# Kernel tuning notes

Hardware: AMD Instinct MI355X
Metric: run time of the kernel (lower is better)

The kernel has to match this reference:

```python
import jax, jax.numpy as jnp
import numpy as np

B, C, E, K, HW = 8, 64, 4, 2, 128
LEAK = 0.2      # LeakyReLU slope in gate and experts
CLAMP = 0.8     # InvBlock clamp
EPS = 1e-5      # InstanceNorm eps


def _conv(x, w, b, pad):
    # x: [B,Ci,H,W], w: [Co,Ci,kh,kw] (OIHW)
    y = jax.lax.conv_general_dilated(x, w, (1, 1), [(pad, pad), (pad, pad)],
                                     dimension_numbers=('NCHW', 'OIHW', 'NCHW'))
    return y + b[None, :, None, None]


def _inorm(x, g, b):
    # InstanceNorm2d: per-sample, per-channel over H,W; biased variance
    m = x.mean(axis=(2, 3), keepdims=True)
    v = x.var(axis=(2, 3), keepdims=True)
    return (x - m) / jnp.sqrt(v + EPS) * g[None, :, None, None] + b[None, :, None, None]


def _hin(x, w1, b1, nw, nb, w2, b2):
    # HinResBlock with relu_slope=1 (d=1 passed by InvBlock) -> activations are identity
    r = _conv(x, w1, b1, 1)
    h1, h2 = jnp.split(r, 2, axis=1)
    r = jnp.concatenate([_inorm(h1, nw, nb), h2], axis=1)
    r = _conv(r, w2, b2, 1)
    return x + r


def setup_inputs() -> dict:
    key = jax.random.key(0)
    ks = jax.random.split(key, 20)
    s = 0.05
    Ch = C // 2
    inp = {
        'x': jax.random.normal(ks[0], (B, 2 * C, HW, HW), jnp.float32),
        # invertible 1x1 conv weight [2C, 2C]
        'winv': jax.random.normal(ks[1], (2 * C, 2 * C), jnp.float32) * s,
        # stacked HinResBlock params for F (idx 0), G (idx 1), H (idx 2)
        'blk_w1': jax.random.normal(ks[2], (3, C, C, 3, 3), jnp.float32) * s,
        'blk_b1': jax.random.normal(ks[3], (3, C), jnp.float32) * s,
        'blk_nw': jnp.ones((3, Ch), jnp.float32),
        'blk_nb': jnp.zeros((3, Ch), jnp.float32),
        'blk_w2': jax.random.normal(ks[4], (3, C, C, 3, 3), jnp.float32) * s,
        'blk_b2': jax.random.normal(ks[5], (3, C), jnp.float32) * s,
        # fuse 1x1 conv 2C -> C
        'fuse_w': jax.random.normal(ks[6], (C, 2 * C, 1, 1), jnp.float32) * s,
        'fuse_b': jax.random.normal(ks[7], (C,), jnp.float32) * s,
        # gate: fc0 (noise) random; fc1 weight zero-init per source, bias random
        'gw0': jax.random.normal(ks[8], (E, C), jnp.float32) * s,
        'gb0': jax.random.normal(ks[9], (E,), jnp.float32) * s,
        'gw1': jnp.zeros((E, C), jnp.float32),
        'gb1': jax.random.normal(ks[10], (E,), jnp.float32) * s,
        # stacked expert ConvProce params
        'ew1': jax.random.normal(ks[11], (E, C, C, 3, 3), jnp.float32) * s,
        'eb1': jax.random.normal(ks[12], (E, C), jnp.float32) * s,
        'ew2': jax.random.normal(ks[13], (E, C, C, 3, 3), jnp.float32) * s,
        'eb2': jax.random.normal(ks[14], (E, C), jnp.float32) * s,
    }
    return inp


def _forward(x, winv, blk_w1, blk_b1, blk_nw, blk_nb, blk_w2, blk_b2,
             fuse_w, fuse_b, gw0, gb0, gw1, gb1, ew1, eb1, ew2, eb2):
    # --- pre_fuse: InvBlock(2C, C) then 1x1 conv 2C->C ---
    z = jnp.einsum('oi,bihw->bohw', winv, x)  # invertible 1x1 conv (logdet unused)
    x1, x2 = z[:, :C], z[:, C:]
    hin = lambda i, h: _hin(h, blk_w1[i], blk_b1[i], blk_nw[i], blk_nb[i], blk_w2[i], blk_b2[i])
    y1 = x1 + hin(0, x2)                         # F
    s = CLAMP * (jax.nn.sigmoid(hin(2, y1)) * 2.0 - 1.0)  # H
    y2 = x2 * jnp.exp(s) + hin(1, y1)            # G
    xf = _conv(jnp.concatenate([y1, y2], axis=1), fuse_w, fuse_b, 0)  # [B,C,H,W]

    # --- gate ---
    g = jnp.max(xf, axis=(2, 3)) + jnp.mean(xf, axis=(2, 3))  # [B,C]
    lg = jax.nn.leaky_relu(g @ gw1.T + gb1, LEAK)             # [B,E]
    noise = jax.nn.softplus(g @ gw0.T + gb0)
    nm = noise.mean(axis=1, keepdims=True)
    ns = jnp.std(noise, axis=1, ddof=1, keepdims=True)        # torch.std is unbiased
    norm_noise = (noise - nm) / ns
    _, idx = jax.lax.top_k(lg + norm_noise, K)                # [B,K]
    mask = jnp.zeros((B, E), lg.dtype).at[jnp.arange(B)[:, None], idx].set(1.0)
    cof = jax.nn.softmax(jnp.where(mask > 0, lg, -jnp.inf), axis=1)  # [B,E]

    # --- experts: dense weighted combine (non-topk gates are exactly 0) ---
    def expert(w1, b1, w2, b2):
        h = jax.nn.leaky_relu(_conv(xf, w1, b1, 1), LEAK)
        return _conv(h, w2, b2, 1) + xf
    eouts = jax.vmap(expert)(ew1, eb1, ew2, eb2)  # [E,B,C,H,W]
    out = jnp.einsum('ebchw,be->bchw', eouts, cof)
    return out, cof


def reference(x, winv, blk_w1, blk_b1, blk_nw, blk_nb, blk_w2, blk_b2,
              fuse_w, fuse_b, gw0, gb0, gw1, gb1, ew1, eb1, ew2, eb2):
    return _forward(x, winv, blk_w1, blk_b1, blk_nw, blk_nb, blk_w2, blk_b2,
                    fuse_w, fuse_b, gw0, gb0, gw1, gb1, ew1, eb1, ew2, eb2)
```

## Files before the change

### kernel.cpp

```cpp
#include <hip/hip_runtime.h>
#include <cstddef>


#define HW2 16384
typedef short short8 __attribute__((ext_vector_type(8)));
typedef float f32x4 __attribute__((ext_vector_type(4)));
typedef unsigned short ushort_t;
typedef unsigned int uint_t;

enum { M_PLAIN = 0, M_ADD2 = 1, M_SIGEXP = 2, M_COUPLE = 3, M_LRELU = 4 };

__device__ __forceinline__ float bf2f(ushort_t u) {
  return __uint_as_float(((uint_t)u) << 16);
}
__device__ __forceinline__ ushort_t f2bf(float f) {
  uint_t u = __float_as_uint(f);
  u += 0x7fffu + ((u >> 16) & 1u);
  return (ushort_t)(u >> 16);
}
__device__ __forceinline__ uint_t pack2(float a, float b) {
  return (uint_t)f2bf(a) | ((uint_t)f2bf(b) << 16);
}
__device__ __forceinline__ void ld4bf(const ushort_t* p, float* o) {
  uint2 d = *(const uint2*)p;
  o[0] = bf2f((ushort_t)(d.x & 0xffff)); o[1] = bf2f((ushort_t)(d.x >> 16));
  o[2] = bf2f((ushort_t)(d.y & 0xffff)); o[3] = bf2f((ushort_t)(d.y >> 16));
}
__device__ __forceinline__ void st4bf(ushort_t* p, const float* v) {
  uint2 st; st.x = pack2(v[0], v[1]); st.y = pack2(v[2], v[3]);
  *(uint2*)p = st;
}
__device__ __forceinline__ void gload_lds16(const void* g, void* l) {
  __builtin_amdgcn_global_load_lds(
      (const __attribute__((address_space(1))) void*)g,
      (__attribute__((address_space(3))) void*)l, 16, 0, 0);
}

__global__ void wtrans_kernel(const float* __restrict__ bw1, const float* __restrict__ bw2,
                              const float* __restrict__ ew1, const float* __restrict__ ew2,
                              ushort_t* __restrict__ wbuf) {
  int idx = blockIdx.x * 256 + threadIdx.x;
  int ci = idx & 63; int co = (idx >> 6) & 63;
  int rest = idx >> 12;
  int tap = rest % 9; int conv = rest / 9;
  const float* src;
  if (conv < 3)       src = bw1 + (size_t)conv * 36864;
  else if (conv < 6)  src = bw2 + (size_t)(conv - 3) * 36864;
  else if (conv < 10) src = ew1 + (size_t)(conv - 6) * 36864;
  else                src = ew2 + (size_t)(conv - 10) * 36864;
  float v = src[(co * 64 + ci) * 9 + tap];
  int n = co >> 4, col = co & 15;
  int h = ci >> 5, krow = (ci >> 3) & 3, e = ci & 7;
  int pos = conv * 36864 + (((tap * 2 + h) * 4 + n) << 9) + ((col << 2) + krow) * 8 + e;
  wbuf[pos] = f2bf(v);
}

__global__ void cvt_kernel(const float* __restrict__ s, ushort_t* __restrict__ d, int n) {
  int i = blockIdx.x * 256 + threadIdx.x;
  if (i < n) d[i] = f2bf(s[i]);
}

__global__ __launch_bounds__(256) void xtrans_kernel(const float* __restrict__ x,
                                                     ushort_t* __restrict__ xh) {
  int b = blockIdx.y;
  int oct = blockIdx.x >> 6;
  int p = ((blockIdx.x & 63) << 8) + threadIdx.x;
  short8 v;
#pragma unroll
  for (int j = 0; j < 8; ++j)
    v[j] = (short)f2bf(x[((size_t)(b * 128 + oct * 8 + j)) * HW2 + p]);
  *(short8*)(xh + ((size_t)b * HW2 + p) * 128 + oct * 8) = v;
}

template <int MODE, bool INORM>
__global__ __launch_bounds__(256, 2) void conv3_kernel(
    const ushort_t* __restrict__ in, int icstr, int icoff,
    const ushort_t* __restrict__ wgt, const float* __restrict__ bias,
    void* __restrict__ outv, int ocstr, int ocoff,
    const ushort_t* __restrict__ r1, int r1cstr, int r1off,
    const ushort_t* __restrict__ r2, int r2cstr, int r2off,
    const ushort_t* __restrict__ mul, int mcstr, int moff,
    const float* __restrict__ kh, const int* __restrict__ eidx) {
  int b = blockIdx.y;
  if (MODE == M_LRELU) {
    int e = eidx[b * 2 + (int)blockIdx.z];
    wgt += (size_t)(6 + e) * 36864;
    bias += e * 64;
    outv = (void*)((ushort_t*)outv + (size_t)blockIdx.z * 8388608);
  }
  int tile = blockIdx.x;
  int ty0 = (tile >> 3) << 4;
  int tx0 = (tile & 7) << 4;
  int t = threadIdx.x;
  int lane = t & 63, w = t >> 6;

  __shared__ __align__(16) ushort_t sm[2592 * 8];
  char* smb = (char*)sm;

  if (!INORM) {
    for (int j = t; j < 2592; j += 256) {
      int row = j / 144, rem = j - row * 144;
      int xx = rem >> 3;
      int gy = ty0 + row - 1, gx = tx0 + xx - 1;
      if ((unsigned)gy >= 128u || (unsigned)gx >= 128u) {
        short8 z = {0, 0, 0, 0, 0, 0, 0, 0};
        *(short8*)(smb + (j << 4)) = z;
      }
    }
    for (int k = w; k < 41; k += 4) {
      int j = (k << 6) + lane;
      int row = j / 144, rem = j - row * 144;
      int xx = rem >> 3, octS = rem & 7;
      int oct = octS ^ (xx & 7);
      int gy = ty0 + row - 1, gx = tx0 + xx - 1;
      if (j < 2592 && (unsigned)gy < 128u && (unsigned)gx < 128u) {
        const ushort_t* gp =
            in + ((size_t)b * HW2 + (gy << 7) + gx) * icstr + icoff + oct * 8;
        gload_lds16(gp, smb + (k << 10));
      }
    }
  } else {
    short8 v[11];
#pragma unroll
    for (int k = 0; k < 11; ++k) {
      int j = t + (k << 8);
      short8 vv = {0, 0, 0, 0, 0, 0, 0, 0};
      if (j < 2592) {
        int row = j / 144, rem = j - row * 144;
        int xx = rem >> 3, octS = rem & 7;
        int oct = octS ^ (xx & 7);
        int gy = ty0 + row - 1, gx = tx0 + xx - 1;
        if ((unsigned)gy < 128u && (unsigned)gx < 128u) {
          vv = *(const short8*)(in + ((size_t)b * HW2 + (gy << 7) + gx) * icstr + icoff + oct * 8);
          if (oct < 4) {
            const float* khp = kh + (b * 32 + oct * 8) * 2;
#pragma unroll
            for (int jq = 0; jq < 8; ++jq) {
              float f = bf2f((ushort_t)vv[jq]);
              vv[jq] = (short)f2bf(f * khp[jq * 2] + khp[jq * 2 + 1]);
            }
          }
        }
      }
      v[k] = vv;
    }
#pragma unroll
    for (int k = 0; k < 11; ++k) {
      int j = t + (k << 8);
      if (j < 2592) *(short8*)(smb + (j << 4)) = v[k];
    }
  }
  __syncthreads();

  int col = lane & 15, krow = lane >> 4;
  int wofs = ((col << 2) + krow) * 8;
  f32x4 acc[4][4] = {};

#pragma unroll
  for (int tap = 0; tap < 9; ++tap) {
    const int dy = tap / 3, dx = tap - dy * 3;
#pragma unroll
    for (int h = 0; h < 2; ++h) {
      short8 af[4];
      const ushort_t* wbase = wgt + (((tap * 2 + h) * 4) << 9) + wofs;
#pragma unroll
      for (int n = 0; n < 4; ++n) af[n] = *(const short8*)(wbase + (n << 9));
      short8 bfr[4];
#pragma unroll
      for (int s = 0; s < 4; ++s) {
        int row = (w << 2) + s + dy, xx = col + dx;
        bfr[s] = *(const short8*)(smb +
                 (((row * 18 + xx) * 8 + ((h * 4 + krow) ^ (xx & 7))) << 4));
      }
#pragma unroll
      for (int s = 0; s < 4; ++s)
#pragma unroll
        for (int n = 0; n < 4; ++n)
          acc[s][n] = __builtin_amdgcn_mfma_f32_16x16x32_bf16(af[n], bfr[s], acc[s][n], 0, 0, 0);
    }
  }

#pragma unroll
  for (int s = 0; s < 4; ++s) {
    int py = ty0 + (w << 2) + s;
    size_t pix = (size_t)b * HW2 + (py << 7) + tx0 + col;
#pragma unroll
    for (int n = 0; n < 4; ++n) {
      int cb = n * 16 + krow * 4;
      float v[4];
#pragma unroll
      for (int r = 0; r < 4; ++r) v[r] = acc[s][n][r] + bias[cb + r];
      if (MODE == M_PLAIN) {
        st4bf((ushort_t*)outv + pix * ocstr + ocoff + cb, v);
      } else if (MODE == M_ADD2) {
        float a[4], bb[4];
        ld4bf(r1 + pix * r1cstr + r1off + cb, a);
        ld4bf(r2 + pix * r2cstr + r2off + cb, bb);
#pragma unroll
        for (int r = 0; r < 4; ++r) v[r] += a[r] + bb[r];
        st4bf((ushort_t*)outv + pix * ocstr + ocoff + cb, v);
      } else if (MODE == M_SIGEXP) {
        float a[4];
        ld4bf(r1 + pix * r1cstr + r1off + cb, a);
#pragma unroll
        for (int r = 0; r < 4; ++r) {
          float tt = v[r] + a[r];
          float sg = 1.f / (1.f + __expf(-tt));
          v[r] = __expf(1.6f * sg - 0.8f);
        }
        st4bf((ushort_t*)outv + pix * ocstr + ocoff + cb, v);
      } else if (MODE == M_COUPLE) {
        float a[4], bb[4], mm[4];
        ld4bf(r1 + pix * r1cstr + r1off + cb, a);
        ld4bf(r2 + pix * r2cstr + r2off + cb, bb);
        ld4bf(mul + pix * mcstr + moff + cb, mm);
#pragma unroll
        for (int r = 0; r < 4; ++r) v[r] += a[r] + bb[r] * mm[r];
        st4bf((ushort_t*)outv + pix * ocstr + ocoff + cb, v);
      } else if (MODE == M_LRELU) {
#pragma unroll
        for (int r = 0; r < 4; ++r) v[r] = v[r] > 0.f ? v[r] : 0.2f * v[r];
        st4bf((ushort_t*)outv + pix * ocstr + ocoff + cb, v);
      }
    }
  }
}

__global__ __launch_bounds__(256) void efin_kernel(
    const ushort_t* __restrict__ hbase,
    const ushort_t* __restrict__ xf,
    const ushort_t* __restrict__ wgt14,
    const float* __restrict__ eb2,
    const int* __restrict__ eidx, const float* __restrict__ cof,
    float* __restrict__ out) {
  int b = blockIdx.y;
  int tile = blockIdx.x;
  int ty0 = (tile >> 3) << 3;
  int tx0 = (tile & 7) << 4;
  int t = threadIdx.x, lane = t & 63, w = t >> 6;
  int col = lane & 15, krow = lane >> 4;
  __shared__ __align__(16) ushort_t sm[1440 * 8];
  char* smb = (char*)sm;
  int e0 = eidx[b * 2], e1 = eidx[b * 2 + 1];
  float c0 = cof[b * 4 + e0], c1 = cof[b * 4 + e1];
  int wofs = ((col << 2) + krow) * 8;
  f32x4 acc[2][4] = {};

  for (int s = 0; s < 2; ++s) {
    float cs = s ? c1 : c0;
    const ushort_t* hsrc = hbase + (size_t)s * 8388608;
    const ushort_t* wgt = wgt14 + (size_t)(10 + (s ? e1 : e0)) * 36864;
    if (s) __syncthreads();
    short8 v[6];
#pragma unroll
    for (int k = 0; k < 6; ++k) {
      int j = t + (k << 8);
      short8 vv = {0, 0, 0, 0, 0, 0, 0, 0};
      if (j < 1440) {
        int row = j / 144, rem = j - row * 144;
        int xx = rem >> 3, octS = rem & 7;
        int oct = octS ^ (xx & 7);
        int gy = ty0 + row - 1, gx = tx0 + xx - 1;
        if ((unsigned)gy < 128u && (unsigned)gx < 128u) {
          vv = *(const short8*)(hsrc + ((size_t)b * HW2 + (gy << 7) + gx) * 64 + oct * 8);
#pragma unroll
          for (int jq = 0; jq < 8; ++jq)
            vv[jq] = (short)f2bf(bf2f((ushort_t)vv[jq]) * cs);
        }
      }
      v[k] = vv;
    }
#pragma unroll
    for (int k = 0; k < 6; ++k) {
      int j = t + (k << 8);
      if (j < 1440) *(short8*)(smb + (j << 4)) = v[k];
    }
    __syncthreads();
#pragma unroll
    for (int tap = 0; tap < 9; ++tap) {
      const int dy = tap / 3, dx = tap - dy * 3;
#pragma unroll
      for (int h = 0; h < 2; ++h) {
        short8 af[4];
        const ushort_t* wbase = wgt + (((tap * 2 + h) * 4) << 9) + wofs;
#pragma unroll
        for (int n = 0; n < 4; ++n) af[n] = *(const short8*)(wbase + (n << 9));
        short8 bfr[2];
#pragma unroll
        for (int ss = 0; ss < 2; ++ss) {
          int row = (w << 1) + ss + dy, xx = col + dx;
          bfr[ss] = *(const short8*)(smb +
                   (((row * 18 + xx) * 8 + ((h * 4 + krow) ^ (xx & 7))) << 4));
        }
#pragma unroll
        for (int ss = 0; ss < 2; ++ss)
#pragma unroll
          for (int n = 0; n < 4; ++n)
            acc[ss][n] = __builtin_amdgcn_mfma_f32_16x16x32_bf16(af[n], bfr[ss], acc[ss][n], 0, 0, 0);
      }
    }
  }

#pragma unroll
  for (int ss = 0; ss < 2; ++ss) {
    int py = ty0 + (w << 1) + ss;
    size_t pnh = (size_t)b * HW2 + (py << 7) + tx0 + col;
#pragma unroll
    for (int n = 0; n < 4; ++n) {
      int cb = n * 16 + krow * 4;
      float xv[4];
      ld4bf(xf + pnh * 64 + cb, xv);
#pragma unroll
      for (int r = 0; r < 4; ++r) {
        int c = cb + r;
        float bb = c0 * eb2[e0 * 64 + c] + c1 * eb2[e1 * 64 + c];
        out[(((size_t)b * 64 + c) << 14) + (py << 7) + tx0 + col] =
            acc[ss][n][r] + bb + xv[r];
      }
    }
  }
}

template <int NF>
__global__ __launch_bounds__(256, 2) void mm1_kernel(
    const ushort_t* __restrict__ in, int icstr,
    const ushort_t* __restrict__ wgt, const float* __restrict__ bias,
    ushort_t* __restrict__ out, int ocstr) {
  int b = blockIdx.y;
  int p0 = blockIdx.x << 7;
  int t = threadIdx.x, lane = t & 63, w = t >> 6;
  int col = lane & 15, krow = lane >> 4;
  size_t pixb = (size_t)b * HW2 + p0 + w * 32;
  short8 bfr[4][2];
#pragma unroll
  for (int kk = 0; kk < 4; ++kk)
#pragma unroll
    for (int s = 0; s < 2; ++s)
      bfr[kk][s] = *(const short8*)(in + (pixb + s * 16 + col) * icstr + kk * 32 + krow * 8);
  f32x4 acc[2][NF] = {};
#pragma unroll
  for (int kk = 0; kk < 4; ++kk) {
#pragma unroll
    for (int n = 0; n < NF; ++n) {
      short8 af = *(const short8*)(wgt + (n * 16 + col) * 128 + kk * 32 + krow * 8);
#pragma unroll
      for (int s = 0; s < 2; ++s)
        acc[s][n] = __builtin_amdgcn_mfma_f32_16x16x32_bf16(af, bfr[kk][s], acc[s][n], 0, 0, 0);
    }
  }
#pragma unroll
  for (int s = 0; s < 2; ++s) {
    size_t pix = pixb + s * 16 + col;
#pragma unroll
    for (int n = 0; n < NF; ++n) {
      int cb = n * 16 + krow * 4;
      float v[4];
#pragma unroll
      for (int r = 0; r < 4; ++r) v[r] = acc[s][n][r] + (bias ? bias[cb + r] : 0.f);
      st4bf(out + pix * ocstr + cb, v);
    }
  }
}

__global__ __launch_bounds__(256) void ireduce_kernel(const ushort_t* __restrict__ h,
                                                      float* __restrict__ part) {
  int b = blockIdx.y, chunk = blockIdx.x, t = threadIdx.x;
  int c = t & 31, g = t >> 5;
  float s = 0.f, q = 0.f;
  const ushort_t* base = h + ((size_t)b * HW2 + chunk * 512) * 64 + c;
  for (int i = 0; i < 64; ++i) {
    float f = bf2f(base[(g + i * 8) * 64]);
    s += f; q += f * f;
  }
  __shared__ float ls[8][32], lq[8][32];
  ls[g][c] = s; lq[g][c] = q;
  __syncthreads();
  if (t < 32) {
    float S = 0.f, Q = 0.f;
    for (int gg = 0; gg < 8; ++gg) { S += ls[gg][t]; Q += lq[gg][t]; }
    float* pp = part + ((b * 32 + chunk) * 32 + t) * 2;
    pp[0] = S; pp[1] = Q;
  }
}

__global__ void istat_kernel(const float* __restrict__ part, const float* __restrict__ nw,
                             const float* __restrict__ nb, float* __restrict__ kh) {
  int t = threadIdx.x; if (t >= 256) return;
  int b = t >> 5, c = t & 31;
  float S = 0.f, Q = 0.f;
  for (int ch = 0; ch < 32; ++ch) {
    const float* pp = part + ((b * 32 + ch) * 32 + c) * 2;
    S += pp[0]; Q += pp[1];
  }
  float m = S * (1.f / 16384.f);
  float var = Q * (1.f / 16384.f) - m * m;
  float k = nw[c] * rsqrtf(var + 1e-5f);
  kh[(b * 32 + c) * 2] = k;
  kh[(b * 32 + c) * 2 + 1] = nb[c] - m * k;
}

__global__ __launch_bounds__(256) void preduce_kernel(const ushort_t* __restrict__ xf,
                                                      float* __restrict__ part2) {
  int b = blockIdx.y, chunk = blockIdx.x, t = threadIdx.x;
  int c = t & 63, g = t >> 6;
  float s = 0.f, mx = -3.4e38f;
  const ushort_t* base = xf + ((size_t)b * HW2 + chunk * 512) * 64 + c;
  for (int i = 0; i < 128; ++i) {
    float f = bf2f(base[(g + i * 4) * 64]);
    s += f; mx = fmaxf(mx, f);
  }
  __shared__ float ls[4][64], lm[4][64];
  ls[g][c] = s; lm[g][c] = mx;
  __syncthreads();
  if (t < 64) {
    float S = ls[0][t] + ls[1][t] + ls[2][t] + ls[3][t];
    float M = fmaxf(fmaxf(lm[0][t], lm[1][t]), fmaxf(lm[2][t], lm[3][t]));
    float* pp = part2 + ((b * 32 + chunk) * 64 + t) * 2;
    pp[0] = S; pp[1] = M;
  }
}

__global__ void pool2_kernel(const float* __restrict__ part2, float* __restrict__ g) {
  int t = blockIdx.x * blockDim.x + threadIdx.x;
  if (t >= 512) return;
  int b = t >> 6, c = t & 63;
  float S = 0.f, M = -3.4e38f;
  for (int ch = 0; ch < 32; ++ch) {
    const float* pp = part2 + ((b * 32 + ch) * 64 + c) * 2;
    S += pp[0]; M = fmaxf(M, pp[1]);
  }
  g[t] = M + S * (1.f / 16384.f);
}

__global__ void gate_kernel(const float* __restrict__ g, const float* __restrict__ gw0,
                            const float* __restrict__ gb0, const float* __restrict__ gw1,
                            const float* __restrict__ gb1, float* __restrict__ cof,
                            int* __restrict__ eidx) {
  int b = threadIdx.x;
  if (b >= 8) return;
  float lg[4], noise[4];
  for (int e = 0; e < 4; ++e) {
    float a0 = gb0[e], a1 = gb1[e];
    for (int c = 0; c < 64; ++c) {
      float gv = g[b * 64 + c];
      a0 += gv * gw0[e * 64 + c];
      a1 += gv * gw1[e * 64 + c];
    }
    lg[e] = a1 > 0.f ? a1 : 0.2f * a1;
    noise[e] = fmaxf(a0, 0.f) + log1pf(expf(-fabsf(a0)));
  }
  float nm = 0.25f * (noise[0] + noise[1] + noise[2] + noise[3]);
  float vs = 0.f;
  for (int e = 0; e < 4; ++e) { float d = noise[e] - nm; vs += d * d; }
  float ns = sqrtf(vs / 3.f);
  float sc[4];
  for (int e = 0; e < 4; ++e) sc[e] = lg[e] + (noise[e] - nm) / ns;
  int i1 = 0;
  for (int e = 1; e < 4; ++e) if (sc[e] > sc[i1]) i1 = e;
  int i2 = -1;
  for (int e = 0; e < 4; ++e) if (e != i1 && (i2 < 0 || sc[e] > sc[i2])) i2 = e;
  float mx = fmaxf(lg[i1], lg[i2]);
  float e1 = expf(lg[i1] - mx), e2 = expf(lg[i2] - mx);
  float d = e1 + e2;
  for (int e = 0; e < 4; ++e) cof[b * 4 + e] = 0.f;
  cof[b * 4 + i1] = e1 / d;
  cof[b * 4 + i2] = e2 / d;
  eidx[b * 2] = i1;
  eidx[b * 2 + 1] = i2;
}

extern "C" void kernel_launch(void* const* d_in, const int* in_sizes, int n_in,
                              void* d_out, int out_size, void* d_ws, size_t ws_size,
                              hipStream_t stream) {
  const float* x    = (const float*)d_in[0];
  const float* winv = (const float*)d_in[1];
  const float* w1   = (const float*)d_in[2];
  const float* b1   = (const float*)d_in[3];
  const float* nw   = (const float*)d_in[4];
  const float* nb   = (const float*)d_in[5];
  const float* w2   = (const float*)d_in[6];
  const float* b2   = (const float*)d_in[7];
  const float* fw   = (const float*)d_in[8];
  const float* fb   = (const float*)d_in[9];
  const float* gw0  = (const float*)d_in[10];
  const float* gb0  = (const float*)d_in[11];
  const float* gw1  = (const float*)d_in[12];
  const float* gb1  = (const float*)d_in[13];
  const float* ew1  = (const float*)d_in[14];
  const float* eb1  = (const float*)d_in[15];
  const float* ew2  = (const float*)d_in[16];
  const float* eb2  = (const float*)d_in[17];

  char* W = (char*)d_ws;
  ushort_t* A    = (ushort_t*)(W);
  ushort_t* Bz   = (ushort_t*)(W + 33554432);
  ushort_t* Ch   = (ushort_t*)(W + 67108864);
  ushort_t* Dx   = (ushort_t*)(W + 83886080);
  ushort_t* w3   = (ushort_t*)(W + 100663296);
  ushort_t* wmm  = (ushort_t*)(W + 101695488);
  ushort_t* wfu  = (ushort_t*)(W + 101728256);
  float* part1 = (float*)(W + 101744640);
  float* kh    = (float*)(W + 101810176);
  float* part2 = (float*)(W + 101812224);
  float* gbuf  = (float*)(W + 101943296);
  int*   eidx  = (int*)(W + 101945344);

  float* out = (float*)d_out;
  float* cof = out + (size_t)8 * 64 * HW2;

  const int WS3 = 36864;
  dim3 cg1(128, 8), cg3(64, 8), rg(32, 8);

  wtrans_kernel<<<2016, 256, 0, stream>>>(w1, w2, ew1, ew2, w3);
  cvt_kernel<<<64, 256, 0, stream>>>(winv, wmm, 16384);
  cvt_kernel<<<32, 256, 0, stream>>>(fw, wfu, 8192);
  xtrans_kernel<<<dim3(1024, 8), 256, 0, stream>>>(x, A);

  mm1_kernel<8><<<cg1, 256, 0, stream>>>(A, 128, wmm, nullptr, Bz, 128);

  conv3_kernel<M_PLAIN, false><<<cg3, 256, 0, stream>>>(Bz, 128, 64, w3 + 0 * WS3, b1,
      Ch, 64, 0, nullptr,0,0, nullptr,0,0, nullptr,0,0, kh, nullptr);
  ireduce_kernel<<<rg, 256, 0, stream>>>(Ch, part1);
  istat_kernel<<<1, 256, 0, stream>>>(part1, nw, nb, kh);
  conv3_kernel<M_ADD2, true><<<cg3, 256, 0, stream>>>(Ch, 64, 0, w3 + 3 * WS3, b2,
      A, 128, 0, Bz, 128, 64, Bz, 128, 0, nullptr,0,0, kh, nullptr);

  conv3_kernel<M_PLAIN, false><<<cg3, 256, 0, stream>>>(A, 128, 0, w3 + 2 * WS3, b1 + 128,
      Ch, 64, 0, nullptr,0,0, nullptr,0,0, nullptr,0,0, kh, nullptr);
  ireduce_kernel<<<rg, 256, 0, stream>>>(Ch, part1);
  istat_kernel<<<1, 256, 0, stream>>>(part1, nw + 64, nb + 64, kh);
  conv3_kernel<M_SIGEXP, true><<<cg3, 256, 0, stream>>>(Ch, 64, 0, w3 + 5 * WS3, b2 + 128,
      Dx, 64, 0, A, 128, 0, nullptr,0,0, nullptr,0,0, kh, nullptr);

  conv3_kernel<M_PLAIN, false><<<cg3, 256, 0, stream>>>(A, 128, 0, w3 + 1 * WS3, b1 + 64,
      Ch, 64, 0, nullptr,0,0, nullptr,0,0, nullptr,0,0, kh, nullptr);
  ireduce_kernel<<<rg, 256, 0, stream>>>(Ch, part1);
  istat_kernel<<<1, 256, 0, stream>>>(part1, nw + 32, nb + 32, kh);
  conv3_kernel<M_COUPLE, true><<<cg3, 256, 0, stream>>>(Ch, 64, 0, w3 + 4 * WS3, b2 + 64,
      A, 128, 64, A, 128, 0, Bz, 128, 64, Dx, 64, 0, kh, nullptr);

  mm1_kernel<4><<<cg1, 256, 0, stream>>>(A, 128, wfu, fb, Dx, 64);

  preduce_kernel<<<rg, 256, 0, stream>>>(Dx, part2);
  pool2_kernel<<<2, 256, 0, stream>>>(part2, gbuf);
  gate_kernel<<<1, 64, 0, stream>>>(gbuf, gw0, gb0, gw1, gb1, cof, eidx);

  conv3_kernel<M_LRELU, false><<<dim3(64, 8, 2), 256, 0, stream>>>(Dx, 64, 0, w3, eb1,
      A, 64, 0, nullptr,0,0, nullptr,0,0, nullptr,0,0, kh, eidx);
  efin_kernel<<<cg1, 256, 0, stream>>>(A, Dx, w3, eb2, eidx, cof, out);
}
```

Baseline: 476.4 us.

## Fold gate coefficient into expert conv1 epilogue and stage both experts via direct LDS loads

The per-sample gate coefficient is now applied in the first expert conv's LeakyReLU epilogue, so the final kernel no longer rescales its input tile in registers. The final kernel then loads the halo tiles for both selected experts into a doubled shared buffer at once, using direct global-to-LDS loads with zeroed padding, and interleaves the two experts' MFMAs inside a single tap loop. This removes one barrier-separated staging phase and the per-element convert-multiply-convert work. In exchange it doubles shared memory per block, which can lower occupancy, and it changes the bf16 rounding order.

```diff
diff --git a/kernel.cpp b/kernel.cpp
--- a/kernel.cpp
+++ b/kernel.cpp
@@ -80,10 +80,13 @@
     const ushort_t* __restrict__ r1, int r1cstr, int r1off,
     const ushort_t* __restrict__ r2, int r2cstr, int r2off,
     const ushort_t* __restrict__ mul, int mcstr, int moff,
-    const float* __restrict__ kh, const int* __restrict__ eidx) {
+    const float* __restrict__ kh, const int* __restrict__ eidx,
+    const float* __restrict__ cof) {
   int b = blockIdx.y;
+  float cv = 1.f;
   if (MODE == M_LRELU) {
     int e = eidx[b * 2 + (int)blockIdx.z];
+    cv = cof[b * 4 + e];
     wgt += (size_t)(6 + e) * 36864;
     bias += e * 64;
     outv = (void*)((ushort_t*)outv + (size_t)blockIdx.z * 8388608);
@@ -219,7 +222,10 @@
         st4bf((ushort_t*)outv + pix * ocstr + ocoff + cb, v);
       } else if (MODE == M_LRELU) {
 #pragma unroll
-        for (int r = 0; r < 4; ++r) v[r] = v[r] > 0.f ? v[r] : 0.2f * v[r];
+        for (int r = 0; r < 4; ++r) {
+          float lr = v[r] > 0.f ? v[r] : 0.2f * v[r];
+          v[r] = lr * cv;
+        }
         st4bf((ushort_t*)outv + pix * ocstr + ocoff + cb, v);
       }
     }
@@ -239,57 +245,58 @@
   int tx0 = (tile & 7) << 4;
   int t = threadIdx.x, lane = t & 63, w = t >> 6;
   int col = lane & 15, krow = lane >> 4;
-  __shared__ __align__(16) ushort_t sm[1440 * 8];
+  __shared__ __align__(16) ushort_t sm[2880 * 8];
   char* smb = (char*)sm;
   int e0 = eidx[b * 2], e1 = eidx[b * 2 + 1];
   float c0 = cof[b * 4 + e0], c1 = cof[b * 4 + e1];
+
+  for (int j = t; j < 2880; j += 256) {
+    int jj = j >= 1440 ? j - 1440 : j;
+    int row = jj / 144, rem = jj - row * 144;
+    int xx = rem >> 3;
+    int gy = ty0 + row - 1, gx = tx0 + xx - 1;
+    if ((unsigned)gy >= 128u || (unsigned)gx >= 128u) {
+      short8 z = {0, 0, 0, 0, 0, 0, 0, 0};
+      *(short8*)(smb + (j << 4)) = z;
+    }
+  }
+  for (int k = w; k < 45; k += 4) {
+    int j = (k << 6) + lane;
+    int s = j >= 1440 ? 1 : 0;
+    int jj = j - s * 1440;
+    int row = jj / 144, rem = jj - row * 144;
+    int xx = rem >> 3, octS = rem & 7;
+    int oct = octS ^ (xx & 7);
+    int gy = ty0 + row - 1, gx = tx0 + xx - 1;
+    if ((unsigned)gy < 128u && (unsigned)gx < 128u) {
+      const ushort_t* gp = hbase + (size_t)s * 8388608 +
+          ((size_t)b * HW2 + (gy << 7) + gx) * 64 + oct * 8;
+      gload_lds16(gp, smb + (k << 10));
+    }
+  }
+  __syncthreads();
+
   int wofs = ((col << 2) + krow) * 8;
   f32x4 acc[2][4] = {};
-
-  for (int s = 0; s < 2; ++s) {
-    float cs = s ? c1 : c0;
-    const ushort_t* hsrc = hbase + (size_t)s * 8388608;
-    const ushort_t* wgt = wgt14 + (size_t)(10 + (s ? e1 : e0)) * 36864;
-    if (s) __syncthreads();
-    short8 v[6];
-#pragma unroll
-    for (int k = 0; k < 6; ++k) {
-      int j = t + (k << 8);
-      short8 vv = {0, 0, 0, 0, 0, 0, 0, 0};
-      if (j < 1440) {
-        int row = j / 144, rem = j - row * 144;
-        int xx = rem >> 3, octS = rem & 7;
-        int oct = octS ^ (xx & 7);
-        int gy = ty0 + row - 1, gx = tx0 + xx - 1;
-        if ((unsigned)gy < 128u && (unsigned)gx < 128u) {
-          vv = *(const short8*)(hsrc + ((size_t)b * HW2 + (gy << 7) + gx) * 64 + oct * 8);
-#pragma unroll
-          for (int jq = 0; jq < 8; ++jq)
-            vv[jq] = (short)f2bf(bf2f((ushort_t)vv[jq]) * cs);
-        }
-      }
-      v[k] = vv;
-    }
-#pragma unroll
-    for (int k = 0; k < 6; ++k) {
-      int j = t + (k << 8);
-      if (j < 1440) *(short8*)(smb + (j << 4)) = v[k];
-    }
-    __syncthreads();
-#pragma unroll
-    for (int tap = 0; tap < 9; ++tap) {
-      const int dy = tap / 3, dx = tap - dy * 3;
-#pragma unroll
-      for (int h = 0; h < 2; ++h) {
+  const ushort_t* wg0 = wgt14 + (size_t)(10 + e0) * 36864;
+  const ushort_t* wg1 = wgt14 + (size_t)(10 + e1) * 36864;
+
+#pragma unroll
+  for (int tap = 0; tap < 9; ++tap) {
+    const int dy = tap / 3, dx = tap - dy * 3;
+#pragma unroll
+    for (int h = 0; h < 2; ++h) {
+#pragma unroll
+      for (int s = 0; s < 2; ++s) {
+        const ushort_t* wbase = (s ? wg1 : wg0) + (((tap * 2 + h) * 4) << 9) + wofs;
         short8 af[4];
-        const ushort_t* wbase = wgt + (((tap * 2 + h) * 4) << 9) + wofs;
 #pragma unroll
         for (int n = 0; n < 4; ++n) af[n] = *(const short8*)(wbase + (n << 9));
         short8 bfr[2];
 #pragma unroll
         for (int ss = 0; ss < 2; ++ss) {
           int row = (w << 1) + ss + dy, xx = col + dx;
-          bfr[ss] = *(const short8*)(smb +
+          bfr[ss] = *(const short8*)(smb + s * 23040 +
                    (((row * 18 + xx) * 8 + ((h * 4 + krow) ^ (xx & 7))) << 4));
         }
 #pragma unroll
@@ -519,25 +526,25 @@
   mm1_kernel<8><<<cg1, 256, 0, stream>>>(A, 128, wmm, nullptr, Bz, 128);
 
   conv3_kernel<M_PLAIN, false><<<cg3, 256, 0, stream>>>(Bz, 128, 64, w3 + 0 * WS3, b1,
-      Ch, 64, 0, nullptr,0,0, nullptr,0,0, nullptr,0,0, kh, nullptr);
+      Ch, 64, 0, nullptr,0,0, nullptr,0,0, nullptr,0,0, kh, nullptr, nullptr);
   ireduce_kernel<<<rg, 256, 0, stream>>>(Ch, part1);
   istat_kernel<<<1, 256, 0, stream>>>(part1, nw, nb, kh);
   conv3_kernel<M_ADD2, true><<<cg3, 256, 0, stream>>>(Ch, 64, 0, w3 + 3 * WS3, b2,
-      A, 128, 0, Bz, 128, 64, Bz, 128, 0, nullptr,0,0, kh, nullptr);
+      A, 128, 0, Bz, 128, 64, Bz, 128, 0, nullptr,0,0, kh, nullptr, nullptr);
 
   conv3_kernel<M_PLAIN, false><<<cg3, 256, 0, stream>>>(A, 128, 0, w3 + 2 * WS3, b1 + 128,
-      Ch, 64, 0, nullptr,0,0, nullptr,0,0, nullptr,0,0, kh, nullptr);
+      Ch, 64, 0, nullptr,0,0, nullptr,0,0, nullptr,0,0, kh, nullptr, nullptr);
   ireduce_kernel<<<rg, 256, 0, stream>>>(Ch, part1);
   istat_kernel<<<1, 256, 0, stream>>>(part1, nw + 64, nb + 64, kh);
   conv3_kernel<M_SIGEXP, true><<<cg3, 256, 0, stream>>>(Ch, 64, 0, w3 + 5 * WS3, b2 + 128,
-      Dx, 64, 0, A, 128, 0, nullptr,0,0, nullptr,0,0, kh, nullptr);
+      Dx, 64, 0, A, 128, 0, nullptr,0,0, nullptr,0,0, kh, nullptr, nullptr);
 
   conv3_kernel<M_PLAIN, false><<<cg3, 256, 0, stream>>>(A, 128, 0, w3 + 1 * WS3, b1 + 64,
-      Ch, 64, 0, nullptr,0,0, nullptr,0,0, nullptr,0,0, kh, nullptr);
+      Ch, 64, 0, nullptr,0,0, nullptr,0,0, nullptr,0,0, kh, nullptr, nullptr);
   ireduce_kernel<<<rg, 256, 0, stream>>>(Ch, part1);
   istat_kernel<<<1, 256, 0, stream>>>(part1, nw + 32, nb + 32, kh);
   conv3_kernel<M_COUPLE, true><<<cg3, 256, 0, stream>>>(Ch, 64, 0, w3 + 4 * WS3, b2 + 64,
-      A, 128, 64, A, 128, 0, Bz, 128, 64, Dx, 64, 0, kh, nullptr);
+      A, 128, 64, A, 128, 0, Bz, 128, 64, Dx, 64, 0, kh, nullptr, nullptr);
 
   mm1_kernel<4><<<cg1, 256, 0, stream>>>(A, 128, wfu, fb, Dx, 64);
 
@@ -546,6 +553,6 @@
   gate_kernel<<<1, 64, 0, stream>>>(gbuf, gw0, gb0, gw1, gb1, cof, eidx);
 
   conv3_kernel<M_LRELU, false><<<dim3(64, 8, 2), 256, 0, stream>>>(Dx, 64, 0, w3, eb1,
-      A, 64, 0, nullptr,0,0, nullptr,0,0, nullptr,0,0, kh, eidx);
+      A, 64, 0, nullptr,0,0, nullptr,0,0, nullptr,0,0, kh, eidx, cof);
   efin_kernel<<<cg1, 256, 0, stream>>>(A, Dx, w3, eb2, eidx, cof, out);
 }
```

Result: no change. 483.0 us (+1.4%).
